# Performance work log

Hardware: AMD Instinct MI355X
Metric: run time of the kernel (lower is better)

## Reference

```python
import jax, jax.numpy as jnp
import numpy as np

# Gemma-2B style config
B, S, HID = 2, 2048, 2048
H, KH, D = 8, 1, 256          # query heads, kv heads, head_dim
THETA = 10000.0


def setup_inputs() -> dict:
    key = jax.random.key(0)
    ks = jax.random.split(key, 6)
    s = 0.02  # init scale for weights
    return {
        "hidden_states": jax.random.normal(ks[0], (B, S, HID), dtype=jnp.float32),
        "attention_mask": jnp.zeros((B, S), dtype=jnp.float32),  # additive mask over kv axis
        "position_ids": jnp.broadcast_to(jnp.arange(S, dtype=jnp.int32), (B, S)),
        "Wq": jax.random.normal(ks[1], (H * D, HID), dtype=jnp.float32) * s,
        "bq": jnp.zeros((H * D,), dtype=jnp.float32),
        "Wk": jax.random.normal(ks[2], (KH * D, HID), dtype=jnp.float32) * s,
        "bk": jnp.zeros((KH * D,), dtype=jnp.float32),
        "Wv": jax.random.normal(ks[3], (KH * D, HID), dtype=jnp.float32) * s,
        "bv": jnp.zeros((KH * D,), dtype=jnp.float32),
        "Wo": jax.random.normal(ks[4], (HID, H * D), dtype=jnp.float32) * s,
        "bo": jnp.zeros((HID,), dtype=jnp.float32),
    }


def _rope(x, position_ids):
    # x: [b, s, h, d]; rotate-half RoPE per head, computed in fp32 as in the module.
    half = D // 2
    inv_freq = 1.0 / (THETA ** (jnp.arange(0, D, 2, dtype=jnp.float32) / D))  # [d/2]
    freqs = position_ids.astype(jnp.float32)[:, :, None] * inv_freq            # [b, s, d/2]
    cos = jnp.cos(freqs)[:, :, None, :]  # [b, s, 1, d/2]
    sin = jnp.sin(freqs)[:, :, None, :]
    x1, x2 = x[..., :half], x[..., half:]
    return jnp.concatenate([cos * x1 - sin * x2, sin * x1 + cos * x2], axis=-1).astype(x.dtype)


def reference(hidden_states, attention_mask, position_ids, Wq, bq, Wk, bk, Wv, bv, Wo, bo):
    b, s, _ = hidden_states.shape
    q = (hidden_states @ Wq.T + bq).reshape(b, s, H, D)
    k = (hidden_states @ Wk.T + bk).reshape(b, s, KH, D)
    v = (hidden_states @ Wv.T + bv).reshape(b, s, KH, D)
    q = _rope(q, position_ids)
    k = _rope(k, position_ids)
    # GQA: broadcast the KV heads across query-head groups
    groups = H // KH
    k = jnp.repeat(k, groups, axis=2)  # [b, s, H, D]
    v = jnp.repeat(v, groups, axis=2)
    scores = jnp.einsum('bnhd,bmhd->bhnm', q, k) * (D ** -0.5)  # [b, H, s, s]
    scores = scores + attention_mask[:, None, None, :]
    attn = jax.nn.softmax(scores, axis=-1)  # dropout p=0.0 -> identity
    out = jnp.einsum('bhnm,bmhd->bnhd', attn, v).reshape(b, s, H * D)
    out = out @ Wo.T + bo
    return (out, attn)
```

## Files before the change

### kernel.cpp

```cpp
#include <hip/hip_runtime.h>

#define B_ 2
#define S_ 2048
#define HID_ 2048
#define H_ 8
#define D_ 256
#define NQKV 2560

typedef unsigned short u16;
typedef __attribute__((ext_vector_type(8))) short bf16x8;
typedef __attribute__((ext_vector_type(4))) float f32x4;

__device__ __forceinline__ u16 f2b(float x) {
    unsigned u = __float_as_uint(x);
    unsigned rb = (u >> 16) & 1u;
    u += 0x7fffu + rb;
    return (u16)(u >> 16);
}

__device__ __forceinline__ void load_lds16(const u16* g, u16* l) {
    __builtin_amdgcn_global_load_lds(
        (const __attribute__((address_space(1))) void*)g,
        (__attribute__((address_space(3))) void*)l, 16, 0, 0);
}

__global__ __launch_bounds__(256) void cvt_bf16(const float* __restrict__ in,
                                                u16* __restrict__ out, int n) {
    int i = (blockIdx.x * 256 + threadIdx.x) * 4;
    if (i >= n) return;
    float4 f = *(const float4*)(in + i);
    union { u16 u[4]; uint2 v; } pk;
    pk.u[0] = f2b(f.x); pk.u[1] = f2b(f.y); pk.u[2] = f2b(f.z); pk.u[3] = f2b(f.w);
    *(uint2*)(out + i) = pk.v;
}

__global__ __launch_bounds__(256) void concat_bias(const float* __restrict__ bq,
                                                   const float* __restrict__ bk,
                                                   const float* __restrict__ bv,
                                                   float* __restrict__ dst) {
    int i = blockIdx.x * 256 + threadIdx.x;
    if (i >= NQKV) return;
    float v;
    if (i < H_ * D_) v = bq[i];
    else if (i < H_ * D_ + D_) v = bk[i - H_ * D_];
    else v = bv[i - H_ * D_ - D_];
    dst[i] = v;
}

__global__ __launch_bounds__(256) void rope_kernel(const float* __restrict__ x,
                                                   int rowStride, int colOff,
                                                   const int* __restrict__ pos_ids,
                                                   u16* __restrict__ out, int nHeads) {
    int idx = blockIdx.x * 256 + threadIdx.x;
    int d   = idx & 127;
    int tmp = idx >> 7;
    int h   = tmp % nHeads;
    int n   = tmp / nHeads;
    int pos = pos_ids[n];
    float ang = (float)pos * expf(-(float)d * (9.210340371976184f / 128.0f));
    float s, c;
    sincosf(ang, &s, &c);
    size_t src = (size_t)n * rowStride + colOff + (size_t)h * D_;
    float x1 = x[src + d], x2 = x[src + d + 128];
    size_t dst = ((size_t)n * nHeads + h) * D_;
    out[dst + d]       = f2b(c * x1 - s * x2);
    out[dst + d + 128] = f2b(s * x1 + c * x2);
}

__global__ __launch_bounds__(256) void transpose_v(const float* __restrict__ v,
                                                   int rowStride, int colOff,
                                                   u16* __restrict__ vT) {
    __shared__ float t[32][33];
    int b = blockIdx.z;
    int s0 = blockIdx.x * 32, d0 = blockIdx.y * 32;
    int tx = threadIdx.x, ty = threadIdx.y;
#pragma unroll
    for (int i = 0; i < 4; ++i)
        t[ty + i * 8][tx] = v[((size_t)b * S_ + s0 + ty + i * 8) * rowStride + colOff + d0 + tx];
    __syncthreads();
#pragma unroll
    for (int i = 0; i < 4; ++i)
        vT[(size_t)b * D_ * S_ + (size_t)(d0 + ty + i * 8) * S_ + s0 + tx] = f2b(t[tx][ty + i * 8]);
}

__global__ __launch_bounds__(512, 2) void score_softmax(
    const u16* __restrict__ q_b, const u16* __restrict__ k_b,
    const float* __restrict__ mask, float* __restrict__ attn,
    u16* __restrict__ attn_b) {
    __shared__ __align__(16) u16 qs[32 * 256];
    __shared__ float redm[8][16], reds[8][16];

    const int z = blockIdx.z;
    const int bb = z >> 3, hh = z & 7;
    const int n0 = blockIdx.x * 32;
    const int tid = threadIdx.x;
    const int lane = tid & 63, wave = tid >> 6;
    const int l15 = lane & 15, quad = lane >> 4;
    const int rg = wave >> 2, cg = wave & 3;

    const u16* qsrc = q_b + (((size_t)bb * S_ + n0) * H_ + hh) * D_;
#pragma unroll
    for (int i = 0; i < 2; ++i) {
        int c = i * 512 + tid;
        int row = c >> 5, sg = c & 31;
        int g = sg ^ (row & 7);
        load_lds16(qsrc + (size_t)row * (H_ * D_) + g * 8,
                   qs + (size_t)(i * 512 + wave * 64) * 8);
    }

    f32x4 acc[32];
#pragma unroll
    for (int ct = 0; ct < 32; ++ct)
#pragma unroll
        for (int r = 0; r < 4; ++r) acc[ct][r] = 0.f;

    __syncthreads();

    bf16x8 av[8];
    const int rr = rg * 16 + l15;
#pragma unroll
    for (int kk = 0; kk < 8; ++kk)
        av[kk] = *(const bf16x8*)&qs[rr * 256 + (((kk * 4 + quad) ^ (rr & 7)) * 8)];

    const u16* kb = k_b + (size_t)bb * S_ * D_ + (size_t)(cg * 512 + l15) * D_ + quad * 8;
#pragma unroll
    for (int ct = 0; ct < 32; ++ct) {
        const u16* kr = kb + (size_t)ct * 16 * D_;
        bf16x8 bv[8];
#pragma unroll
        for (int kk = 0; kk < 8; ++kk) bv[kk] = *(const bf16x8*)(kr + kk * 32);
#pragma unroll
        for (int kk = 0; kk < 8; ++kk)
            acc[ct] = __builtin_amdgcn_mfma_f32_16x16x32_bf16(av[kk], bv[kk], acc[ct], 0, 0, 0);
    }

    const float sc = 0.0625f;
    const float* maskb = mask + (size_t)bb * S_ + cg * 512 + l15;
    float mx[4] = {-3.4e38f, -3.4e38f, -3.4e38f, -3.4e38f};
#pragma unroll
    for (int ct = 0; ct < 32; ++ct) {
        float mkv = maskb[ct * 16];
#pragma unroll
        for (int r = 0; r < 4; ++r) {
            float xv = acc[ct][r] * sc + mkv;
            acc[ct][r] = xv;
            mx[r] = fmaxf(mx[r], xv);
        }
    }
#pragma unroll
    for (int off = 1; off < 16; off <<= 1)
#pragma unroll
        for (int r = 0; r < 4; ++r) mx[r] = fmaxf(mx[r], __shfl_xor(mx[r], off));
    if (l15 == 0) {
#pragma unroll
        for (int r = 0; r < 4; ++r) redm[wave][quad * 4 + r] = mx[r];
    }
    __syncthreads();
    float fm[4], sm[4];
#pragma unroll
    for (int r = 0; r < 4; ++r) {
        int rw = quad * 4 + r;
        fm[r] = fmaxf(fmaxf(redm[rg * 4 + 0][rw], redm[rg * 4 + 1][rw]),
                      fmaxf(redm[rg * 4 + 2][rw], redm[rg * 4 + 3][rw]));
        sm[r] = 0.f;
    }
#pragma unroll
    for (int ct = 0; ct < 32; ++ct)
#pragma unroll
        for (int r = 0; r < 4; ++r) {
            float e = expf(acc[ct][r] - fm[r]);
            acc[ct][r] = e;
            sm[r] += e;
        }
#pragma unroll
    for (int off = 1; off < 16; off <<= 1)
#pragma unroll
        for (int r = 0; r < 4; ++r) sm[r] += __shfl_xor(sm[r], off);
    if (l15 == 0) {
#pragma unroll
        for (int r = 0; r < 4; ++r) reds[wave][quad * 4 + r] = sm[r];
    }
    __syncthreads();

    size_t obase = ((size_t)(bb * H_ + hh) * S_ + n0 + rg * 16 + quad * 4) * S_
                 + cg * 512 + l15;
#pragma unroll
    for (int r = 0; r < 4; ++r) {
        int rw = quad * 4 + r;
        float inv = 1.f / (reds[rg * 4 + 0][rw] + reds[rg * 4 + 1][rw] +
                           reds[rg * 4 + 2][rw] + reds[rg * 4 + 3][rw]);
        float* ao = attn + obase + (size_t)r * S_;
#pragma unroll
        for (int ct = 0; ct < 32; ++ct) {
            float p = acc[ct][r] * inv;
            ao[ct * 16] = p;
            acc[ct][r] = p;
        }
    }
    if (attn_b) {
        u16* ab = attn_b + obase;
#pragma unroll
        for (int r = 0; r < 4; ++r) {
            u16* abr = ab + (size_t)r * S_;
#pragma unroll
            for (int ct = 0; ct < 32; ++ct) abr[ct * 16] = f2b(acc[ct][r]);
        }
    }
}

#define TILE_M 128
#define TILE_N 128
#define TILE_K 32

template <bool C_IS_BF16>
__global__ __launch_bounds__(256, 2) void gemm_async(
    const u16* __restrict__ Ap, const u16* __restrict__ Bp, void* __restrict__ Cp,
    const float* __restrict__ bias, int lda, int ldb, int ldc, int K,
    long sAb, long sAh, long sBb, long sBh, long sCb, long sCh, int numH) {
    __shared__ __align__(16) u16 As[TILE_M * TILE_K];
    __shared__ __align__(16) u16 Bs[TILE_N * TILE_K];

    int z = blockIdx.z;
    int bb = z / numH, hh = z % numH;
    const u16* Ab = Ap + (long)bb * sAb + (long)hh * sAh;
    const u16* Bb = Bp + (long)bb * sBb + (long)hh * sBh;
    long cOff = (long)bb * sCb + (long)hh * sCh;

    const int m0 = blockIdx.y * TILE_M;
    const int n0 = blockIdx.x * TILE_N;
    const int tid = threadIdx.x;
    const int lane = tid & 63, wave = tid >> 6;
    const int l15 = lane & 15, quad = lane >> 4;
    const int waveM = wave >> 1, waveN = wave & 1;

    f32x4 acc[4][4];
#pragma unroll
    for (int mt = 0; mt < 4; ++mt)
#pragma unroll
        for (int nt = 0; nt < 4; ++nt)
#pragma unroll
            for (int r = 0; r < 4; ++r) acc[mt][nt][r] = 0.f;

    int rowS[2], colS[2];
    u16 *lA[2], *lB[2];
#pragma unroll
    for (int i = 0; i < 2; ++i) {
        int c = i * 256 + tid;
        rowS[i] = c >> 2;
        colS[i] = (((c & 3) ^ ((rowS[i] >> 1) & 3)) * 8);
        lA[i] = As + (size_t)(i * 256 + wave * 64) * 8;
        lB[i] = Bs + (size_t)(i * 256 + wave * 64) * 8;
    }

    for (int k0 = 0; k0 < K; k0 += TILE_K) {
#pragma unroll
        for (int i = 0; i < 2; ++i) {
            load_lds16(Ab + (size_t)(m0 + rowS[i]) * lda + k0 + colS[i], lA[i]);
            load_lds16(Bb + (size_t)(n0 + rowS[i]) * ldb + k0 + colS[i], lB[i]);
        }
        __syncthreads();

        bf16x8 av[4], bv[4];
#pragma unroll
        for (int t = 0; t < 4; ++t) {
            int ra = waveM * 64 + t * 16 + l15;
            av[t] = *(bf16x8*)&As[ra * TILE_K + ((quad ^ ((ra >> 1) & 3)) * 8)];
            int rb = waveN * 64 + t * 16 + l15;
            bv[t] = *(bf16x8*)&Bs[rb * TILE_K + ((quad ^ ((rb >> 1) & 3)) * 8)];
        }
#pragma unroll
        for (int mt = 0; mt < 4; ++mt)
#pragma unroll
            for (int nt = 0; nt < 4; ++nt)
                acc[mt][nt] = __builtin_amdgcn_mfma_f32_16x16x32_bf16(av[mt], bv[nt],
                                                                      acc[mt][nt], 0, 0, 0);
        __syncthreads();
    }

#pragma unroll
    for (int mt = 0; mt < 4; ++mt) {
        int row = m0 + waveM * 64 + mt * 16 + quad * 4;
#pragma unroll
        for (int nt = 0; nt < 4; ++nt) {
            int col = n0 + waveN * 64 + nt * 16 + l15;
            float bia = bias ? bias[col] : 0.f;
#pragma unroll
            for (int r = 0; r < 4; ++r) {
                float val = acc[mt][nt][r] + bia;
                if constexpr (C_IS_BF16)
                    ((u16*)Cp)[cOff + (size_t)(row + r) * ldc + col] = f2b(val);
                else
                    ((float*)Cp)[cOff + (size_t)(row + r) * ldc + col] = val;
            }
        }
    }
}

#define LDSK 40
__global__ __launch_bounds__(256, 2) void gemm_slow_f32a(
    const float* __restrict__ Ap, const u16* __restrict__ Bp, u16* __restrict__ Cp,
    int lda, int ldb, int ldc, int K,
    long sAb, long sAh, long sBb, long sBh, long sCb, long sCh, int numH) {
    __shared__ __align__(16) u16 As[TILE_M * LDSK];
    __shared__ __align__(16) u16 Bs[TILE_N * LDSK];
    int z = blockIdx.z;
    int bb = z / numH, hh = z % numH;
    const float* Af = Ap + (long)bb * sAb + (long)hh * sAh;
    const u16* Bb = Bp + (long)bb * sBb + (long)hh * sBh;
    long cOff = (long)bb * sCb + (long)hh * sCh;
    const int m0 = blockIdx.y * TILE_M, n0 = blockIdx.x * TILE_N;
    const int tid = threadIdx.x;
    const int lane = tid & 63, wave = tid >> 6;
    const int l15 = lane & 15, quad = lane >> 4;
    const int waveM = wave >> 1, waveN = wave & 1;
    f32x4 acc[4][4];
#pragma unroll
    for (int mt = 0; mt < 4; ++mt)
#pragma unroll
        for (int nt = 0; nt < 4; ++nt)
#pragma unroll
            for (int r = 0; r < 4; ++r) acc[mt][nt][r] = 0.f;
    for (int k0 = 0; k0 < K; k0 += TILE_K) {
#pragma unroll
        for (int i = 0; i < 2; ++i) {
            int c = tid + i * 256;
            int row = c >> 2, col = (c & 3) * 8;
            const float* src = Af + (size_t)(m0 + row) * lda + k0 + col;
            float4 f0 = *(const float4*)src;
            float4 f1 = *(const float4*)(src + 4);
            union { u16 u[8]; uint4 v; } pk;
            pk.u[0] = f2b(f0.x); pk.u[1] = f2b(f0.y); pk.u[2] = f2b(f0.z); pk.u[3] = f2b(f0.w);
            pk.u[4] = f2b(f1.x); pk.u[5] = f2b(f1.y); pk.u[6] = f2b(f1.z); pk.u[7] = f2b(f1.w);
            *(uint4*)&As[row * LDSK + col] = pk.v;
            *(uint4*)&Bs[row * LDSK + col] =
                *(const uint4*)(Bb + (size_t)(n0 + row) * ldb + k0 + col);
        }
        __syncthreads();
        bf16x8 av[4], bv[4];
#pragma unroll
        for (int t = 0; t < 4; ++t) {
            av[t] = *(bf16x8*)&As[(waveM * 64 + t * 16 + l15) * LDSK + quad * 8];
            bv[t] = *(bf16x8*)&Bs[(waveN * 64 + t * 16 + l15) * LDSK + quad * 8];
        }
#pragma unroll
        for (int mt = 0; mt < 4; ++mt)
#pragma unroll
            for (int nt = 0; nt < 4; ++nt)
                acc[mt][nt] = __builtin_amdgcn_mfma_f32_16x16x32_bf16(av[mt], bv[nt],
                                                                      acc[mt][nt], 0, 0, 0);
        __syncthreads();
    }
#pragma unroll
    for (int mt = 0; mt < 4; ++mt) {
        int row = m0 + waveM * 64 + mt * 16 + quad * 4;
#pragma unroll
        for (int nt = 0; nt < 4; ++nt) {
            int col = n0 + waveN * 64 + nt * 16 + l15;
#pragma unroll
            for (int r = 0; r < 4; ++r)
                Cp[cOff + (size_t)(row + r) * ldc + col] = f2b(acc[mt][nt][r]);
        }
    }
}

extern "C" void kernel_launch(void* const* d_in, const int* in_sizes, int n_in,
                              void* d_out, int out_size, void* d_ws, size_t ws_size,
                              hipStream_t stream) {
    const float* hs   = (const float*)d_in[0];
    const float* mask = (const float*)d_in[1];
    const int*   pos  = (const int*)d_in[2];
    const float* Wq = (const float*)d_in[3];
    const float* bq = (const float*)d_in[4];
    const float* Wk = (const float*)d_in[5];
    const float* bk = (const float*)d_in[6];
    const float* Wv = (const float*)d_in[7];
    const float* bv = (const float*)d_in[8];
    const float* Wo = (const float*)d_in[9];
    const float* bo = (const float*)d_in[10];

    float* out  = (float*)d_out;
    float* attn = (float*)d_out + (size_t)B_ * S_ * HID_;

    char* ws = (char*)d_ws;
    size_t need = 0;
    u16* hs_b    = (u16*)(ws);          need += (size_t)B_ * S_ * HID_ * 2;
    u16* Wqkv_b  = (u16*)(ws + need);   need += (size_t)NQKV * HID_ * 2;
    u16* Wo_b    = (u16*)(ws + need);   need += (size_t)HID_ * H_ * D_ * 2;
    float* qkv_f = (float*)(ws + need); need += (size_t)B_ * S_ * NQKV * 4;
    u16* q_b     = (u16*)(ws + need);   need += (size_t)B_ * S_ * H_ * D_ * 2;
    u16* k_b     = (u16*)(ws + need);   need += (size_t)B_ * S_ * D_ * 2;
    u16* vT_b    = (u16*)(ws + need);   need += (size_t)B_ * D_ * S_ * 2;
    float* bqkv  = (float*)(ws + need); need += (size_t)NQKV * 4 + 4096;
    need &= ~(size_t)255;
    u16* attn_b  = (u16*)(ws + need);
    size_t need_big = need + (size_t)B_ * H_ * S_ * S_ * 2;
    bool big = ws_size >= need_big;
    u16* ctx_b = hs_b;

    cvt_bf16<<<dim3((B_ * S_ * HID_) / 1024), 256, 0, stream>>>(hs, hs_b, B_ * S_ * HID_);
    cvt_bf16<<<dim3((H_ * D_ * HID_) / 1024), 256, 0, stream>>>(Wq, Wqkv_b, H_ * D_ * HID_);
    cvt_bf16<<<dim3((D_ * HID_) / 1024), 256, 0, stream>>>(Wk, Wqkv_b + (size_t)H_ * D_ * HID_, D_ * HID_);
    cvt_bf16<<<dim3((D_ * HID_) / 1024), 256, 0, stream>>>(Wv, Wqkv_b + (size_t)(H_ * D_ + D_) * HID_, D_ * HID_);
    cvt_bf16<<<dim3((HID_ * H_ * D_) / 1024), 256, 0, stream>>>(Wo, Wo_b, HID_ * H_ * D_);
    concat_bias<<<dim3((NQKV + 255) / 256), 256, 0, stream>>>(bq, bk, bv, bqkv);

    gemm_async<false><<<dim3(NQKV / TILE_N, (B_ * S_) / TILE_M, 1), 256, 0, stream>>>(
        hs_b, Wqkv_b, qkv_f, bqkv, HID_, HID_, NQKV, HID_,
        0, 0, 0, 0, 0, 0, 1);

    rope_kernel<<<dim3((B_ * S_ * H_ * 128) / 256), 256, 0, stream>>>(
        qkv_f, NQKV, 0, pos, q_b, H_);
    rope_kernel<<<dim3((B_ * S_ * 1 * 128) / 256), 256, 0, stream>>>(
        qkv_f, NQKV, H_ * D_, pos, k_b, 1);
    transpose_v<<<dim3(S_ / 32, D_ / 32, B_), dim3(32, 8), 0, stream>>>(
        qkv_f, NQKV, H_ * D_ + D_, vT_b);

    score_softmax<<<dim3(S_ / 32, 1, B_ * H_), 512, 0, stream>>>(
        q_b, k_b, mask, attn, big ? attn_b : nullptr);

    if (big) {
        gemm_async<true><<<dim3(D_ / TILE_N, S_ / TILE_M, B_ * H_), 256, 0, stream>>>(
            attn_b, vT_b, ctx_b, nullptr, S_, S_, H_ * D_, S_,
            (long)H_ * S_ * S_, (long)S_ * S_,
            (long)D_ * S_, 0,
            (long)S_ * H_ * D_, D_,
            H_);
    } else {
        gemm_slow_f32a<<<dim3(D_ / TILE_N, S_ / TILE_M, B_ * H_), 256, 0, stream>>>(
            attn, vT_b, ctx_b, S_, S_, H_ * D_, S_,
            (long)H_ * S_ * S_, (long)S_ * S_,
            (long)D_ * S_, 0,
            (long)S_ * H_ * D_, D_,
            H_);
    }

    gemm_async<false><<<dim3(HID_ / TILE_N, (B_ * S_) / TILE_M, 1), 256, 0, stream>>>(
        ctx_b, Wo_b, out, bo, H_ * D_, H_ * D_, HID_, H_ * D_,
        0, 0, 0, 0, 0, 0, 1);
}
```

Measured before the change: 857.0 us.

## Stage K tiles through LDS in score_softmax with 16-row query blocks

```diff
diff --git a/kernel.cpp b/kernel.cpp
--- a/kernel.cpp
+++ b/kernel.cpp
@@ -83,29 +83,39 @@
         vT[(size_t)b * D_ * S_ + (size_t)(d0 + ty + i * 8) * S_ + s0 + tx] = f2b(t[tx][ty + i * 8]);
 }
 
-__global__ __launch_bounds__(512, 2) void score_softmax(
+__global__ __launch_bounds__(256, 2) void score_softmax(
     const u16* __restrict__ q_b, const u16* __restrict__ k_b,
     const float* __restrict__ mask, float* __restrict__ attn,
     u16* __restrict__ attn_b) {
-    __shared__ __align__(16) u16 qs[32 * 256];
-    __shared__ float redm[8][16], reds[8][16];
+    __shared__ __align__(16) u16 qs[16 * 256];
+    __shared__ __align__(16) u16 ks[64 * 256];
+    __shared__ float redm[4][16], reds[4][16];
 
     const int z = blockIdx.z;
     const int bb = z >> 3, hh = z & 7;
-    const int n0 = blockIdx.x * 32;
+    const int n0 = blockIdx.x * 16;
     const int tid = threadIdx.x;
     const int lane = tid & 63, wave = tid >> 6;
     const int l15 = lane & 15, quad = lane >> 4;
-    const int rg = wave >> 2, cg = wave & 3;
 
     const u16* qsrc = q_b + (((size_t)bb * S_ + n0) * H_ + hh) * D_;
 #pragma unroll
     for (int i = 0; i < 2; ++i) {
-        int c = i * 512 + tid;
+        int c = i * 256 + tid;
         int row = c >> 5, sg = c & 31;
         int g = sg ^ (row & 7);
         load_lds16(qsrc + (size_t)row * (H_ * D_) + g * 8,
-                   qs + (size_t)(i * 512 + wave * 64) * 8);
+                   qs + (size_t)(i * 256 + wave * 64) * 8);
+    }
+
+    const u16* kbase = k_b + (size_t)bb * S_ * D_;
+#pragma unroll
+    for (int j = 0; j < 8; ++j) {
+        int c = j * 256 + tid;
+        int row = c >> 5, sg = c & 31;
+        int g = sg ^ (row & 7);
+        load_lds16(kbase + (size_t)row * D_ + g * 8,
+                   ks + (size_t)(j * 256 + wave * 64) * 8);
     }
 
     f32x4 acc[32];
@@ -117,29 +127,40 @@
     __syncthreads();
 
     bf16x8 av[8];
-    const int rr = rg * 16 + l15;
 #pragma unroll
     for (int kk = 0; kk < 8; ++kk)
-        av[kk] = *(const bf16x8*)&qs[rr * 256 + (((kk * 4 + quad) ^ (rr & 7)) * 8)];
-
-    const u16* kb = k_b + (size_t)bb * S_ * D_ + (size_t)(cg * 512 + l15) * D_ + quad * 8;
+        av[kk] = *(const bf16x8*)&qs[l15 * 256 + (((kk * 4 + quad) ^ (l15 & 7)) * 8)];
+
+#pragma unroll
+    for (int t = 0; t < 32; ++t) {
+        bf16x8 bv[8];
+        const int rb = wave * 16 + l15;
+#pragma unroll
+        for (int kk = 0; kk < 8; ++kk)
+            bv[kk] = *(const bf16x8*)&ks[rb * 256 + (((kk * 4 + quad) ^ (rb & 7)) * 8)];
+#pragma unroll
+        for (int kk = 0; kk < 8; ++kk)
+            acc[t] = __builtin_amdgcn_mfma_f32_16x16x32_bf16(av[kk], bv[kk], acc[t], 0, 0, 0);
+        if (t < 31) {
+            __syncthreads();
+#pragma unroll
+            for (int j = 0; j < 8; ++j) {
+                int c = j * 256 + tid;
+                int row = c >> 5, sg = c & 31;
+                int g = sg ^ (row & 7);
+                load_lds16(kbase + (size_t)((t + 1) * 64 + row) * D_ + g * 8,
+                           ks + (size_t)(j * 256 + wave * 64) * 8);
+            }
+            __syncthreads();
+        }
+    }
+
+    const float sc = 0.0625f;
+    const float* maskb = mask + (size_t)bb * S_ + wave * 16 + l15;
+    float mx[4] = {-3.4e38f, -3.4e38f, -3.4e38f, -3.4e38f};
 #pragma unroll
     for (int ct = 0; ct < 32; ++ct) {
-        const u16* kr = kb + (size_t)ct * 16 * D_;
-        bf16x8 bv[8];
-#pragma unroll
-        for (int kk = 0; kk < 8; ++kk) bv[kk] = *(const bf16x8*)(kr + kk * 32);
-#pragma unroll
-        for (int kk = 0; kk < 8; ++kk)
-            acc[ct] = __builtin_amdgcn_mfma_f32_16x16x32_bf16(av[kk], bv[kk], acc[ct], 0, 0, 0);
-    }
-
-    const float sc = 0.0625f;
-    const float* maskb = mask + (size_t)bb * S_ + cg * 512 + l15;
-    float mx[4] = {-3.4e38f, -3.4e38f, -3.4e38f, -3.4e38f};
-#pragma unroll
-    for (int ct = 0; ct < 32; ++ct) {
-        float mkv = maskb[ct * 16];
+        float mkv = maskb[ct * 64];
 #pragma unroll
         for (int r = 0; r < 4; ++r) {
             float xv = acc[ct][r] * sc + mkv;
@@ -160,8 +181,8 @@
 #pragma unroll
     for (int r = 0; r < 4; ++r) {
         int rw = quad * 4 + r;
-        fm[r] = fmaxf(fmaxf(redm[rg * 4 + 0][rw], redm[rg * 4 + 1][rw]),
-                      fmaxf(redm[rg * 4 + 2][rw], redm[rg * 4 + 3][rw]));
+        fm[r] = fmaxf(fmaxf(redm[0][rw], redm[1][rw]),
+                      fmaxf(redm[2][rw], redm[3][rw]));
         sm[r] = 0.f;
     }
 #pragma unroll
@@ -182,18 +203,17 @@
     }
     __syncthreads();
 
-    size_t obase = ((size_t)(bb * H_ + hh) * S_ + n0 + rg * 16 + quad * 4) * S_
-                 + cg * 512 + l15;
+    size_t obase = ((size_t)(bb * H_ + hh) * S_ + n0 + quad * 4) * S_
+                 + wave * 16 + l15;
 #pragma unroll
     for (int r = 0; r < 4; ++r) {
         int rw = quad * 4 + r;
-        float inv = 1.f / (reds[rg * 4 + 0][rw] + reds[rg * 4 + 1][rw] +
-                           reds[rg * 4 + 2][rw] + reds[rg * 4 + 3][rw]);
+        float inv = 1.f / (reds[0][rw] + reds[1][rw] + reds[2][rw] + reds[3][rw]);
         float* ao = attn + obase + (size_t)r * S_;
 #pragma unroll
         for (int ct = 0; ct < 32; ++ct) {
             float p = acc[ct][r] * inv;
-            ao[ct * 16] = p;
+            ao[ct * 64] = p;
             acc[ct][r] = p;
         }
     }
@@ -203,7 +223,7 @@
         for (int r = 0; r < 4; ++r) {
             u16* abr = ab + (size_t)r * S_;
 #pragma unroll
-            for (int ct = 0; ct < 32; ++ct) abr[ct * 16] = f2b(acc[ct][r]);
+            for (int ct = 0; ct < 32; ++ct) abr[ct * 64] = f2b(acc[ct][r]);
         }
     }
 }
@@ -415,7 +435,7 @@
     transpose_v<<<dim3(S_ / 32, D_ / 32, B_), dim3(32, 8), 0, stream>>>(
         qkv_f, NQKV, H_ * D_ + D_, vT_b);
 
-    score_softmax<<<dim3(S_ / 32, 1, B_ * H_), 512, 0, stream>>>(
+    score_softmax<<<dim3(S_ / 16, 1, B_ * H_), 256, 0, stream>>>(
         q_b, k_b, mask, attn, big ? attn_b : nullptr);
 
     if (big) {
```

New measurement: 741.9 us. 1.16x faster.
